# Optimization experiments

Measured on AMD Instinct MI355X. Metric: run time of the kernel, lower is better.

Reference implementation:

```python
import jax, jax.numpy as jnp
import numpy as np
from jax import lax

B = 16384  # batch; original torch module runs unbatched (1,5,27), we vectorize over B


def _conv(x, w, b, ph):
    # NCHW conv with kernel (kh,1), padding (ph,0), stride 1
    y = lax.conv_general_dilated(x, w, (1, 1), [(ph, ph), (0, 0)],
                                 dimension_numbers=('NCHW', 'OIHW', 'NCHW'))
    return y + b[None, :, None, None]


def _sl(x, w, b):
    # Semi_Linear: shared Linear applied over every (channel, height) slice ->
    # algebraically a single batched matmul on the last axis. w: (out,in)
    return jnp.einsum('bchw,ow->bcho', x, w) + b


def setup_inputs() -> dict:
    key = jax.random.key(0)
    ks = iter(jax.random.split(key, 40))
    def p(shape):
        return jax.random.normal(next(ks), shape, jnp.float32) * 0.05
    d = dict(
        x=jax.random.normal(next(ks), (B, 1, 5, 27), jnp.float32),
        w0a=p((5, 1, 3, 1)), b0a=p((5,)),
        wl0=p((18, 27)), bl0=p((18,)),
        w0b=p((25, 5, 3, 1)), b0b=p((25,)),
        w0c=p((25, 1, 1, 1)), b0c=p((25,)),
        wr0=p((18, 27)), br0=p((18,)),
        w1=p((75, 25, 2, 1)), b1=p((75,)),
        wl1=p((10, 18)), bl1=p((10,)),
        w2=p((125, 75, 2, 1)), b2=p((125,)),
        wa=p((125, 25, 3, 1)), ba=p((125,)),
        wra=p((10, 18)), bra=p((10,)),
        w0=p((300, 125, 2, 1)), b0=p((300,)),
        wl2=p((5, 10)), bl2=p((5,)),
        w0b2=p((512, 300, 2, 1)), b0b2=p((512,)),
        w0c2=p((512, 125, 3, 1)), b0c2=p((512,)),
        wr02=p((5, 10)), br02=p((5,)),
    )
    return d


def reference(x, w0a, b0a, wl0, bl0, w0b, b0b, w0c, b0c, wr0, br0,
              w1, b1, wl1, bl1, w2, b2, wa, ba, wra, bra,
              w0, b0, wl2, bl2, w0b2, b0b2, w0c2, b0c2, wr02, br02):
    # stage 0
    z = _conv(x, w0a, b0a, 1)                      # (B,5,5,27)
    z = jax.nn.relu(_sl(z, wl0, bl0))              # (B,5,5,18)
    z = _conv(z, w0b, b0b, 1)                      # (B,25,5,18)
    y = _conv(_sl(x, wr0, br0), w0c, b0c, 0)       # (B,25,5,18)
    x1 = z + y
    # stage 1
    z = _conv(x1, w1, b1, 0)                       # (B,75,4,18)
    z = jax.nn.relu(_sl(z, wl1, bl1))              # (B,75,4,10)
    z = _conv(z, w2, b2, 0)                        # (B,125,3,10)
    y = _conv(_sl(x1, wra, bra), wa, ba, 0)        # (B,125,3,10)
    x2 = z + y
    # stage 2
    z = _conv(x2, w0, b0, 0)                       # (B,300,2,10)
    z = jax.nn.relu(_sl(z, wl2, bl2))              # (B,300,2,5)
    z = _conv(z, w0b2, b0b2, 0)                    # (B,512,1,5)
    y = _conv(_sl(x2, wr02, br02), w0c2, b0c2, 0)  # (B,512,1,5)
    return z + y
```

## Files before the change

### kernel.cpp

```cpp
#include <hip/hip_runtime.h>
#include <stdint.h>


#define WB2T_OFF 0
#define WC2T_OFF 307200
#define W0T_OFF  499200
#define W1T_OFF  574200
#define WAT_OFF  577950
#define W2T_OFF  587325
#define WT_TOTAL 606075

__global__ __launch_bounds__(256)
void transpose_w(const float* __restrict__ w1, const float* __restrict__ wa,
                 const float* __restrict__ w2, const float* __restrict__ w0,
                 const float* __restrict__ wb2, const float* __restrict__ wc2,
                 float* __restrict__ ws) {
  int i = blockIdx.x * 256 + threadIdx.x;
  if (i < 3750) {
    int co = i / 50, k = i % 50;
    ws[W1T_OFF + k*75 + co] = w1[i];
  } else if (i < 13125) {
    int j = i - 3750; int co = j / 75, k = j % 75;
    ws[WAT_OFF + k*125 + co] = wa[j];
  } else if (i < 31875) {
    int j = i - 13125; int co = j / 150, k = j % 150;
    ws[W2T_OFF + k*125 + co] = w2[j];
  } else if (i < 106875) {
    int j = i - 31875; int co = j / 250, k = j % 250;
    ws[W0T_OFF + k*300 + co] = w0[j];
  } else if (i < 414075) {
    int j = i - 106875; int co = j / 600, k = j % 600;
    ws[WB2T_OFF + k*512 + co] = wb2[j];
  } else if (i < 606075) {
    int j = i - 414075; int co = j / 375, k = j % 375;
    ws[WC2T_OFF + k*512 + co] = wc2[j];
  }
}

template<int N>
__device__ __forceinline__ void ldrow(float* r, const float* p) {
  #pragma unroll
  for (int i = 0; i < N/4; ++i) {
    float4 q = reinterpret_cast<const float4*>(p)[i];
    r[4*i+0] = q.x; r[4*i+1] = q.y; r[4*i+2] = q.z; r[4*i+3] = q.w;
  }
}
template<int N>
__device__ __forceinline__ void strow(float* p, const float* r) {
  #pragma unroll
  for (int i = 0; i < N/4; ++i) {
    float4 q; q.x = r[4*i+0]; q.y = r[4*i+1]; q.z = r[4*i+2]; q.w = r[4*i+3];
    reinterpret_cast<float4*>(p)[i] = q;
  }
}

#define POOL   10112
#define X1_O   0
#define SX_O   2500
#define Z0A_O  2640
#define Z0SL_O 4500
#define T90_O  5000
#define Z1S_O  4500
#define T2_O   8100
#define X2_O   0
#define T3_O   4500
#define Z2S_O  6500

__global__ __launch_bounds__(256, 2)
void fused_net(const float* __restrict__ xg,
  const float* __restrict__ w0a_, const float* __restrict__ b0a_,
  const float* __restrict__ wl0_, const float* __restrict__ bl0_,
  const float* __restrict__ w0b_, const float* __restrict__ b0b_,
  const float* __restrict__ w0c_, const float* __restrict__ b0c_,
  const float* __restrict__ wr0_, const float* __restrict__ br0_,
  const float* __restrict__ b1_,
  const float* __restrict__ wl1_, const float* __restrict__ bl1_,
  const float* __restrict__ b2_,
  const float* __restrict__ ba_,
  const float* __restrict__ wra_, const float* __restrict__ bra_,
  const float* __restrict__ b0_,
  const float* __restrict__ wl2_, const float* __restrict__ bl2_,
  const float* __restrict__ b0b2_,
  const float* __restrict__ b0c2_,
  const float* __restrict__ wr02_,const float* __restrict__ br02_,
  const float* __restrict__ w1t, const float* __restrict__ wat,
  const float* __restrict__ w2t, const float* __restrict__ w0t,
  const float* __restrict__ wb2t, const float* __restrict__ wc2t,
  float* __restrict__ outg, int Btot)
{
  __shared__ __align__(16) float S[2*POOL];
  const int tid = threadIdx.x;
  const int b0 = blockIdx.x * 2;

  for (int i = tid; i < 270; i += 256) {
    int samp = i / 135, j = i % 135;
    int h = j / 27, w = j % 27;
    float v = 0.f;
    if (b0 + samp < Btot) v = xg[(size_t)(b0 + samp) * 135 + j];
    S[samp*POOL + SX_O + h*28 + w] = v;
  }
  __syncthreads();

  if (tid < 50) {
    int samp = tid / 25, r = tid % 25, co = r / 5, h = r % 5;
    float* P = S + samp*POOL;
    float acc[28];
    float bias = b0a_[co];
    #pragma unroll
    for (int w = 0; w < 28; ++w) acc[w] = bias;
    #pragma unroll
    for (int dh = 0; dh < 3; ++dh) {
      int hi = h + dh - 1;
      if (hi >= 0 && hi < 5) {
        float wf = w0a_[co*3 + dh];
        float row[28]; ldrow<28>(row, P + SX_O + hi*28);
        #pragma unroll
        for (int w = 0; w < 27; ++w) acc[w] += row[w] * wf;
      }
    }
    strow<28>(P + Z0A_O + (co*5 + h)*28, acc);
  }
  __syncthreads();

  if (tid < 180) {
    int samp = tid / 90, r = tid % 90;
    float* P = S + samp*POOL;
    if (r < 75) {
      int c = r / 15, q = r % 15, h = q / 3, o0 = (q % 3) * 6;
      float row[28]; ldrow<28>(row, P + Z0A_O + (c*5 + h)*28);
      float acc[6];
      #pragma unroll
      for (int k = 0; k < 6; ++k) acc[k] = bl0_[o0 + k];
      for (int w = 0; w < 27; ++w) {
        float rv = row[w];
        #pragma unroll
        for (int k = 0; k < 6; ++k) acc[k] += rv * wl0_[(o0 + k)*27 + w];
      }
      float* dst = P + Z0SL_O + (c*5 + h)*20 + o0;
      #pragma unroll
      for (int k = 0; k < 6; ++k) dst[k] = fmaxf(acc[k], 0.f);
    } else {
      int q = r - 75, h = q / 3, o0 = (q % 3) * 6;
      float row[28]; ldrow<28>(row, P + SX_O + h*28);
      float acc[6];
      #pragma unroll
      for (int k = 0; k < 6; ++k) acc[k] = br0_[o0 + k];
      for (int w = 0; w < 27; ++w) {
        float rv = row[w];
        #pragma unroll
        for (int k = 0; k < 6; ++k) acc[k] += rv * wr0_[(o0 + k)*27 + w];
      }
      float* dst = P + T90_O + h*20 + o0;
      #pragma unroll
      for (int k = 0; k < 6; ++k) dst[k] = acc[k];
    }
  }
  __syncthreads();

  if (tid < 250) {
    int samp = tid / 125, r = tid % 125, co = r / 5, h = r % 5;
    float* P = S + samp*POOL;
    float tr[20]; ldrow<20>(tr, P + T90_O + h*20);
    float wc = w0c_[co];
    float base = b0b_[co] + b0c_[co];
    float acc[20];
    #pragma unroll
    for (int o = 0; o < 18; ++o) acc[o] = base + tr[o]*wc;
    acc[18] = 0.f; acc[19] = 0.f;
    #pragma unroll
    for (int dh = 0; dh < 3; ++dh) {
      int hi = h + dh - 1;
      if (hi >= 0 && hi < 5) {
        #pragma unroll
        for (int ci = 0; ci < 5; ++ci) {
          float wgt = w0b_[(co*5 + ci)*3 + dh];
          float row[20]; ldrow<20>(row, P + Z0SL_O + (ci*5 + hi)*20);
          #pragma unroll
          for (int o = 0; o < 18; ++o) acc[o] += row[o] * wgt;
        }
      }
    }
    strow<20>(P + X1_O + (co*5 + h)*20, acc);
  }
  __syncthreads();

  for (int t = tid; t < 850; t += 256) {
    if (t < 600) {
      int samp = t / 300, r = t % 300, co = r / 4, h = r % 4;
      float* P = S + samp*POOL;
      float z1[18];
      float bias = b1_[co];
      #pragma unroll
      for (int w = 0; w < 18; ++w) z1[w] = bias;
      for (int ci = 0; ci < 25; ++ci) {
        float wx = w1t[(ci*2 + 0)*75 + co];
        float wy = w1t[(ci*2 + 1)*75 + co];
        float r0[20], r1[20];
        ldrow<20>(r0, P + X1_O + (ci*5 + h    )*20);
        ldrow<20>(r1, P + X1_O + (ci*5 + h + 1)*20);
        #pragma unroll
        for (int w = 0; w < 18; ++w) z1[w] += r0[w]*wx + r1[w]*wy;
      }
      float out[12];
      #pragma unroll
      for (int o = 0; o < 10; ++o) {
        float acc = bl1_[o];
        #pragma unroll
        for (int w = 0; w < 18; ++w) acc += z1[w] * wl1_[o*18 + w];
        out[o] = fmaxf(acc, 0.f);
      }
      out[10] = 0.f; out[11] = 0.f;
      strow<12>(P + Z1S_O + (co*4 + h)*12, out);
    } else {
      int q = t - 600;
      int samp = q / 125, r = q % 125, c = r / 5, h = r % 5;
      float* P = S + samp*POOL;
      float row[20]; ldrow<20>(row, P + X1_O + (c*5 + h)*20);
      float out[12];
      #pragma unroll
      for (int o = 0; o < 10; ++o) {
        float acc = bra_[o];
        #pragma unroll
        for (int w = 0; w < 18; ++w) acc += row[w] * wra_[o*18 + w];
        out[o] = acc;
      }
      out[10] = 0.f; out[11] = 0.f;
      strow<12>(P + T2_O + (c*5 + h)*12, out);
    }
  }
  __syncthreads();

  if (tid < 250) {
    int samp = tid / 125, co = tid % 125;
    float* P = S + samp*POOL;
    float acc[3][10];
    float bias = b2_[co] + ba_[co];
    #pragma unroll
    for (int h = 0; h < 3; ++h)
      #pragma unroll
      for (int w = 0; w < 10; ++w) acc[h][w] = bias;
    for (int ci = 0; ci < 25; ++ci) {
      float wf0 = wat[(ci*3 + 0)*125 + co];
      float wf1 = wat[(ci*3 + 1)*125 + co];
      float wf2 = wat[(ci*3 + 2)*125 + co];
      float rr[5][12];
      #pragma unroll
      for (int hh = 0; hh < 5; ++hh) ldrow<12>(rr[hh], P + T2_O + (ci*5 + hh)*12);
      #pragma unroll
      for (int h = 0; h < 3; ++h)
        #pragma unroll
        for (int w = 0; w < 10; ++w)
          acc[h][w] += rr[h][w]*wf0 + rr[h+1][w]*wf1 + rr[h+2][w]*wf2;
    }
    #pragma unroll
    for (int h = 0; h < 3; ++h) {
      float out[12];
      #pragma unroll
      for (int w = 0; w < 10; ++w) out[w] = acc[h][w];
      out[10] = 0.f; out[11] = 0.f;
      strow<12>(P + X2_O + (co*3 + h)*12, out);
    }
  }
  __syncthreads();

  if (tid < 250) {
    int samp = tid / 125, co = tid % 125;
    float* P = S + samp*POOL;
    float acc[3][12];
    #pragma unroll
    for (int h = 0; h < 3; ++h) ldrow<12>(acc[h], P + X2_O + (co*3 + h)*12);
    for (int ci = 0; ci < 75; ++ci) {
      float wx = w2t[(ci*2 + 0)*125 + co];
      float wy = w2t[(ci*2 + 1)*125 + co];
      float rr[4][12];
      #pragma unroll
      for (int hh = 0; hh < 4; ++hh) ldrow<12>(rr[hh], P + Z1S_O + (ci*4 + hh)*12);
      #pragma unroll
      for (int h = 0; h < 3; ++h)
        #pragma unroll
        for (int w = 0; w < 10; ++w)
          acc[h][w] += rr[h][w]*wx + rr[h+1][w]*wy;
    }
    #pragma unroll
    for (int h = 0; h < 3; ++h) strow<12>(P + X2_O + (co*3 + h)*12, acc[h]);
  }
  __syncthreads();

  for (int t = tid; t < 400; t += 256) {
    if (t < 150) {
      int samp = t / 75, cot = t % 75;
      int co = cot * 4;
      float* P = S + samp*POOL;
      float acc[4][2][10];
      #pragma unroll
      for (int j = 0; j < 4; ++j) {
        float bb = b0_[co + j];
        #pragma unroll
        for (int h = 0; h < 2; ++h)
          #pragma unroll
          for (int w = 0; w < 10; ++w) acc[j][h][w] = bb;
      }
      for (int ci = 0; ci < 125; ++ci) {
        float a0[12], a1[12], a2[12];
        ldrow<12>(a0, P + X2_O + (ci*3 + 0)*12);
        ldrow<12>(a1, P + X2_O + (ci*3 + 1)*12);
        ldrow<12>(a2, P + X2_O + (ci*3 + 2)*12);
        float4 wxv = *reinterpret_cast<const float4*>(w0t + (ci*2 + 0)*300 + co);
        float4 wyv = *reinterpret_cast<const float4*>(w0t + (ci*2 + 1)*300 + co);
        float wx[4] = {wxv.x, wxv.y, wxv.z, wxv.w};
        float wy[4] = {wyv.x, wyv.y, wyv.z, wyv.w};
        #pragma unroll
        for (int j = 0; j < 4; ++j)
          #pragma unroll
          for (int w = 0; w < 10; ++w) {
            acc[j][0][w] += a0[w]*wx[j] + a1[w]*wy[j];
            acc[j][1][w] += a1[w]*wx[j] + a2[w]*wy[j];
          }
      }
      #pragma unroll
      for (int j = 0; j < 4; ++j) {
        float out[12];
        #pragma unroll
        for (int h = 0; h < 2; ++h)
          #pragma unroll
          for (int o = 0; o < 5; ++o) {
            float sacc = bl2_[o];
            #pragma unroll
            for (int w = 0; w < 10; ++w) sacc += acc[j][h][w] * wl2_[o*10 + w];
            out[h*5 + o] = fmaxf(sacc, 0.f);
          }
        out[10] = 0.f; out[11] = 0.f;
        strow<12>(P + Z2S_O + (co + j)*12, out);
      }
    } else {
      int q = t - 150;
      int samp = q / 125, c = q % 125;
      float* P = S + samp*POOL;
      float rr[3][12];
      #pragma unroll
      for (int h = 0; h < 3; ++h) ldrow<12>(rr[h], P + X2_O + (c*3 + h)*12);
      float out[16];
      #pragma unroll
      for (int h = 0; h < 3; ++h)
        #pragma unroll
        for (int o = 0; o < 5; ++o) {
          float acc = br02_[o];
          #pragma unroll
          for (int w = 0; w < 10; ++w) acc += rr[h][w] * wr02_[o*10 + w];
          out[h*5 + o] = acc;
        }
      out[15] = 0.f;
      strow<16>(P + T3_O + c*16, out);
    }
  }
  __syncthreads();

  {
    int samp = tid >> 7, coq = tid & 127;
    int co = coq * 4;
    float* P = S + samp*POOL;
    float acc[4][5];
    #pragma unroll
    for (int j = 0; j < 4; ++j) {
      float bb = b0b2_[co + j] + b0c2_[co + j];
      #pragma unroll
      for (int w = 0; w < 5; ++w) acc[j][w] = bb;
    }
    for (int ci = 0; ci < 300; ++ci) {
      float a[12]; ldrow<12>(a, P + Z2S_O + ci*12);
      float4 uxv = *reinterpret_cast<const float4*>(wb2t + (ci*2 + 0)*512 + co);
      float4 uyv = *reinterpret_cast<const float4*>(wb2t + (ci*2 + 1)*512 + co);
      float ux[4] = {uxv.x, uxv.y, uxv.z, uxv.w};
      float uy[4] = {uyv.x, uyv.y, uyv.z, uyv.w};
      #pragma unroll
      for (int j = 0; j < 4; ++j)
        #pragma unroll
        for (int w = 0; w < 5; ++w)
          acc[j][w] += a[w]*ux[j] + a[5 + w]*uy[j];
    }
    for (int ci = 0; ci < 125; ++ci) {
      float t3[16]; ldrow<16>(t3, P + T3_O + ci*16);
      float4 u0v = *reinterpret_cast<const float4*>(wc2t + (ci*3 + 0)*512 + co);
      float4 u1v = *reinterpret_cast<const float4*>(wc2t + (ci*3 + 1)*512 + co);
      float4 u2v = *reinterpret_cast<const float4*>(wc2t + (ci*3 + 2)*512 + co);
      float u0[4] = {u0v.x, u0v.y, u0v.z, u0v.w};
      float u1[4] = {u1v.x, u1v.y, u1v.z, u1v.w};
      float u2[4] = {u2v.x, u2v.y, u2v.z, u2v.w};
      #pragma unroll
      for (int j = 0; j < 4; ++j)
        #pragma unroll
        for (int w = 0; w < 5; ++w)
          acc[j][w] += t3[w]*u0[j] + t3[5 + w]*u1[j] + t3[10 + w]*u2[j];
    }
    if (b0 + samp < Btot) {
      float* ob = outg + (size_t)(b0 + samp) * 2560 + co*5;
      float flat[20];
      #pragma unroll
      for (int j = 0; j < 4; ++j)
        #pragma unroll
        for (int w = 0; w < 5; ++w) flat[j*5 + w] = acc[j][w];
      strow<20>(ob, flat);
    }
  }
}

extern "C" void kernel_launch(void* const* d_in, const int* in_sizes, int n_in,
                              void* d_out, int out_size, void* d_ws, size_t ws_size,
                              hipStream_t stream) {
  (void)in_sizes; (void)n_in; (void)ws_size;
  const float* p[31];
  for (int i = 0; i < 31; ++i) p[i] = (const float*)d_in[i];
  float* ws = (float*)d_ws;

  transpose_w<<<(WT_TOTAL + 255) / 256, 256, 0, stream>>>(
      p[11] , p[17] , p[15] , p[21] ,
      p[25] , p[27] , ws);

  int Btot = out_size / 2560;
  int nb = (Btot + 1) >> 1;
  if (nb <= 0) return;
  fused_net<<<nb, 256, 0, stream>>>(
      p[0],
      p[1],  p[2],  p[3],  p[4],  p[5],  p[6],  p[7],  p[8],  p[9],  p[10],
      p[12],
      p[13], p[14],
      p[16],
      p[18],
      p[19], p[20],
      p[22],
      p[23], p[24],
      p[26],
      p[28],
      p[29], p[30],
      ws + W1T_OFF, ws + WAT_OFF, ws + W2T_OFF, ws + W0T_OFF,
      ws + WB2T_OFF, ws + WC2T_OFF,
      (float*)d_out, Btot);
}
```

Baseline: 3.461 ms.

## Reorder kernel-height convs before Semi_Linear to shrink width and fuse stages

Since a (kh,1) conv acts only on channel and height and the Semi_Linear acts only on width, the two commute. Each stage now applies the width-reducing linear first and then runs the conv on the narrower tensor. The conv bias is folded in using precomputed row sums of the linear weights. This cuts FLOPs in the stage-0/1/2 conv-then-linear chains and merges several phases, saving syncs and LDS traffic. The cost is a new shared-memory layout with aliased regions, which needs care to stay race-free.

```diff
diff --git a/kernel.cpp b/kernel.cpp
--- a/kernel.cpp
+++ b/kernel.cpp
@@ -8,12 +8,17 @@
 #define W1T_OFF  574200
 #define WAT_OFF  577950
 #define W2T_OFF  587325
-#define WT_TOTAL 606075
+#define SUM0_OFF 606075
+#define SUM1_OFF 606093
+#define SUM2_OFF 606103
+#define WT_TOTAL 606108
 
 __global__ __launch_bounds__(256)
 void transpose_w(const float* __restrict__ w1, const float* __restrict__ wa,
                  const float* __restrict__ w2, const float* __restrict__ w0,
                  const float* __restrict__ wb2, const float* __restrict__ wc2,
+                 const float* __restrict__ wl0, const float* __restrict__ wl1,
+                 const float* __restrict__ wl2,
                  float* __restrict__ ws) {
   int i = blockIdx.x * 256 + threadIdx.x;
   if (i < 3750) {
@@ -34,6 +39,18 @@
   } else if (i < 606075) {
     int j = i - 414075; int co = j / 375, k = j % 375;
     ws[WC2T_OFF + k*512 + co] = wc2[j];
+  } else if (i < 606093) {
+    int j = i - 606075; float s = 0.f;
+    for (int w = 0; w < 27; ++w) s += wl0[j*27 + w];
+    ws[SUM0_OFF + j] = s;
+  } else if (i < 606103) {
+    int j = i - 606093; float s = 0.f;
+    for (int w = 0; w < 18; ++w) s += wl1[j*18 + w];
+    ws[SUM1_OFF + j] = s;
+  } else if (i < 606108) {
+    int j = i - 606103; float s = 0.f;
+    for (int w = 0; w < 10; ++w) s += wl2[j*10 + w];
+    ws[SUM2_OFF + j] = s;
   }
 }
 
@@ -57,14 +74,16 @@
 #define POOL   10112
 #define X1_O   0
 #define SX_O   2500
-#define Z0A_O  2640
-#define Z0SL_O 4500
-#define T90_O  5000
+#define XS0_O  2640
+#define T90_O  2740
+#define Z0SL_O 2840
+#define X1S_O  2500
 #define Z1S_O  4500
 #define T2_O   8100
 #define X2_O   0
-#define T3_O   4500
-#define Z2S_O  6500
+#define T3_O   8100
+#define X2S_O  4500
+#define Z2S_O  0
 
 __global__ __launch_bounds__(256, 2)
 void fused_net(const float* __restrict__ xg,
@@ -86,6 +105,7 @@
   const float* __restrict__ w1t, const float* __restrict__ wat,
   const float* __restrict__ w2t, const float* __restrict__ w0t,
   const float* __restrict__ wb2t, const float* __restrict__ wc2t,
+  const float* __restrict__ sums,
   float* __restrict__ outg, int Btot)
 {
   __shared__ __align__(16) float S[2*POOL];
@@ -101,64 +121,55 @@
   }
   __syncthreads();
 
+  if (tid < 30) {
+    int samp = tid / 15, r = tid % 15, h = r / 3, o0 = (r % 3) * 6;
+    float* P = S + samp*POOL;
+    float row[28]; ldrow<28>(row, P + SX_O + h*28);
+    float xs[6], t9[6];
+    #pragma unroll
+    for (int k = 0; k < 6; ++k) { xs[k] = 0.f; t9[k] = br0_[o0 + k]; }
+    for (int w = 0; w < 27; ++w) {
+      float rv = row[w];
+      #pragma unroll
+      for (int k = 0; k < 6; ++k) {
+        xs[k] += rv * wl0_[(o0 + k)*27 + w];
+        t9[k] += rv * wr0_[(o0 + k)*27 + w];
+      }
+    }
+    #pragma unroll
+    for (int k = 0; k < 6; ++k) {
+      P[XS0_O + h*20 + o0 + k] = xs[k];
+      P[T90_O + h*20 + o0 + k] = t9[k];
+    }
+  }
+  __syncthreads();
+
   if (tid < 50) {
     int samp = tid / 25, r = tid % 25, co = r / 5, h = r % 5;
     float* P = S + samp*POOL;
-    float acc[28];
-    float bias = b0a_[co];
-    #pragma unroll
-    for (int w = 0; w < 28; ++w) acc[w] = bias;
+    float acc[20];
+    float bc = b0a_[co];
+    #pragma unroll
+    for (int o = 0; o < 18; ++o) acc[o] = bc * sums[o] + bl0_[o];
+    acc[18] = 0.f; acc[19] = 0.f;
     #pragma unroll
     for (int dh = 0; dh < 3; ++dh) {
       int hi = h + dh - 1;
       if (hi >= 0 && hi < 5) {
         float wf = w0a_[co*3 + dh];
-        float row[28]; ldrow<28>(row, P + SX_O + hi*28);
-        #pragma unroll
-        for (int w = 0; w < 27; ++w) acc[w] += row[w] * wf;
-      }
-    }
-    strow<28>(P + Z0A_O + (co*5 + h)*28, acc);
-  }
-  __syncthreads();
-
-  if (tid < 180) {
-    int samp = tid / 90, r = tid % 90;
-    float* P = S + samp*POOL;
-    if (r < 75) {
-      int c = r / 15, q = r % 15, h = q / 3, o0 = (q % 3) * 6;
-      float row[28]; ldrow<28>(row, P + Z0A_O + (c*5 + h)*28);
-      float acc[6];
-      #pragma unroll
-      for (int k = 0; k < 6; ++k) acc[k] = bl0_[o0 + k];
-      for (int w = 0; w < 27; ++w) {
-        float rv = row[w];
-        #pragma unroll
-        for (int k = 0; k < 6; ++k) acc[k] += rv * wl0_[(o0 + k)*27 + w];
-      }
-      float* dst = P + Z0SL_O + (c*5 + h)*20 + o0;
-      #pragma unroll
-      for (int k = 0; k < 6; ++k) dst[k] = fmaxf(acc[k], 0.f);
-    } else {
-      int q = r - 75, h = q / 3, o0 = (q % 3) * 6;
-      float row[28]; ldrow<28>(row, P + SX_O + h*28);
-      float acc[6];
-      #pragma unroll
-      for (int k = 0; k < 6; ++k) acc[k] = br0_[o0 + k];
-      for (int w = 0; w < 27; ++w) {
-        float rv = row[w];
-        #pragma unroll
-        for (int k = 0; k < 6; ++k) acc[k] += rv * wr0_[(o0 + k)*27 + w];
-      }
-      float* dst = P + T90_O + h*20 + o0;
-      #pragma unroll
-      for (int k = 0; k < 6; ++k) dst[k] = acc[k];
-    }
+        float row[20]; ldrow<20>(row, P + XS0_O + hi*20);
+        #pragma unroll
+        for (int o = 0; o < 18; ++o) acc[o] += row[o] * wf;
+      }
+    }
+    #pragma unroll
+    for (int o = 0; o < 18; ++o) acc[o] = fmaxf(acc[o], 0.f);
+    strow<20>(P + Z0SL_O + (co*5 + h)*20, acc);
   }
   __syncthreads();
 
   if (tid < 250) {
-    int samp = tid / 125, r = tid % 125, co = r / 5, h = r % 5;
+    int samp = tid / 125, r = tid % 125, h = r / 25, co = r % 25;
     float* P = S + samp*POOL;
     float tr[20]; ldrow<20>(tr, P + T90_O + h*20);
     float wc = w0c_[co];
@@ -184,48 +195,57 @@
   }
   __syncthreads();
 
-  for (int t = tid; t < 850; t += 256) {
-    if (t < 600) {
-      int samp = t / 300, r = t % 300, co = r / 4, h = r % 4;
-      float* P = S + samp*POOL;
-      float z1[18];
-      float bias = b1_[co];
-      #pragma unroll
-      for (int w = 0; w < 18; ++w) z1[w] = bias;
-      for (int ci = 0; ci < 25; ++ci) {
-        float wx = w1t[(ci*2 + 0)*75 + co];
-        float wy = w1t[(ci*2 + 1)*75 + co];
-        float r0[20], r1[20];
-        ldrow<20>(r0, P + X1_O + (ci*5 + h    )*20);
-        ldrow<20>(r1, P + X1_O + (ci*5 + h + 1)*20);
-        #pragma unroll
-        for (int w = 0; w < 18; ++w) z1[w] += r0[w]*wx + r1[w]*wy;
-      }
+  if (tid < 250) {
+    int samp = tid / 125, r = tid % 125, h = r / 25, c = r % 25;
+    float* P = S + samp*POOL;
+    float row[20]; ldrow<20>(row, P + X1_O + (c*5 + h)*20);
+    float t2[12], x1s[12];
+    #pragma unroll
+    for (int o = 0; o < 10; ++o) {
+      float a = bra_[o], s = 0.f;
+      #pragma unroll
+      for (int w = 0; w < 18; ++w) {
+        a += row[w] * wra_[o*18 + w];
+        s += row[w] * wl1_[o*18 + w];
+      }
+      t2[o] = a; x1s[o] = s;
+    }
+    t2[10] = t2[11] = 0.f; x1s[10] = x1s[11] = 0.f;
+    strow<12>(P + T2_O  + (c*5 + h)*12, t2);
+    strow<12>(P + X1S_O + (c*5 + h)*12, x1s);
+  }
+  __syncthreads();
+
+  for (int t = tid; t < 300; t += 256) {
+    int samp = t / 150, r = t % 150, co = r >> 1, h0 = (r & 1) * 2;
+    float* P = S + samp*POOL;
+    float acc[2][10];
+    float bc = b1_[co];
+    #pragma unroll
+    for (int o = 0; o < 10; ++o) {
+      float b = bc * sums[18 + o] + bl1_[o];
+      acc[0][o] = b; acc[1][o] = b;
+    }
+    for (int ci = 0; ci < 25; ++ci) {
+      float wx = w1t[(ci*2 + 0)*75 + co];
+      float wy = w1t[(ci*2 + 1)*75 + co];
+      float r0[12], r1[12], r2[12];
+      ldrow<12>(r0, P + X1S_O + (ci*5 + h0    )*12);
+      ldrow<12>(r1, P + X1S_O + (ci*5 + h0 + 1)*12);
+      ldrow<12>(r2, P + X1S_O + (ci*5 + h0 + 2)*12);
+      #pragma unroll
+      for (int o = 0; o < 10; ++o) {
+        acc[0][o] += r0[o]*wx + r1[o]*wy;
+        acc[1][o] += r1[o]*wx + r2[o]*wy;
+      }
+    }
+    #pragma unroll
+    for (int hh = 0; hh < 2; ++hh) {
       float out[12];
       #pragma unroll
-      for (int o = 0; o < 10; ++o) {
-        float acc = bl1_[o];
-        #pragma unroll
-        for (int w = 0; w < 18; ++w) acc += z1[w] * wl1_[o*18 + w];
-        out[o] = fmaxf(acc, 0.f);
-      }
+      for (int o = 0; o < 10; ++o) out[o] = fmaxf(acc[hh][o], 0.f);
       out[10] = 0.f; out[11] = 0.f;
-      strow<12>(P + Z1S_O + (co*4 + h)*12, out);
-    } else {
-      int q = t - 600;
-      int samp = q / 125, r = q % 125, c = r / 5, h = r % 5;
-      float* P = S + samp*POOL;
-      float row[20]; ldrow<20>(row, P + X1_O + (c*5 + h)*20);
-      float out[12];
-      #pragma unroll
-      for (int o = 0; o < 10; ++o) {
-        float acc = bra_[o];
-        #pragma unroll
-        for (int w = 0; w < 18; ++w) acc += row[w] * wra_[o*18 + w];
-        out[o] = acc;
-      }
-      out[10] = 0.f; out[11] = 0.f;
-      strow<12>(P + T2_O + (c*5 + h)*12, out);
+      strow<12>(P + Z1S_O + (co*4 + h0 + hh)*12, out);
     }
   }
   __syncthreads();
@@ -252,23 +272,6 @@
         for (int w = 0; w < 10; ++w)
           acc[h][w] += rr[h][w]*wf0 + rr[h+1][w]*wf1 + rr[h+2][w]*wf2;
     }
-    #pragma unroll
-    for (int h = 0; h < 3; ++h) {
-      float out[12];
-      #pragma unroll
-      for (int w = 0; w < 10; ++w) out[w] = acc[h][w];
-      out[10] = 0.f; out[11] = 0.f;
-      strow<12>(P + X2_O + (co*3 + h)*12, out);
-    }
-  }
-  __syncthreads();
-
-  if (tid < 250) {
-    int samp = tid / 125, co = tid % 125;
-    float* P = S + samp*POOL;
-    float acc[3][12];
-    #pragma unroll
-    for (int h = 0; h < 3; ++h) ldrow<12>(acc[h], P + X2_O + (co*3 + h)*12);
     for (int ci = 0; ci < 75; ++ci) {
       float wx = w2t[(ci*2 + 0)*125 + co];
       float wy = w2t[(ci*2 + 1)*125 + co];
@@ -282,75 +285,83 @@
           acc[h][w] += rr[h][w]*wx + rr[h+1][w]*wy;
     }
     #pragma unroll
-    for (int h = 0; h < 3; ++h) strow<12>(P + X2_O + (co*3 + h)*12, acc[h]);
-  }
-  __syncthreads();
-
-  for (int t = tid; t < 400; t += 256) {
-    if (t < 150) {
-      int samp = t / 75, cot = t % 75;
-      int co = cot * 4;
-      float* P = S + samp*POOL;
-      float acc[4][2][10];
-      #pragma unroll
-      for (int j = 0; j < 4; ++j) {
-        float bb = b0_[co + j];
-        #pragma unroll
-        for (int h = 0; h < 2; ++h)
-          #pragma unroll
-          for (int w = 0; w < 10; ++w) acc[j][h][w] = bb;
-      }
-      for (int ci = 0; ci < 125; ++ci) {
-        float a0[12], a1[12], a2[12];
-        ldrow<12>(a0, P + X2_O + (ci*3 + 0)*12);
-        ldrow<12>(a1, P + X2_O + (ci*3 + 1)*12);
-        ldrow<12>(a2, P + X2_O + (ci*3 + 2)*12);
-        float4 wxv = *reinterpret_cast<const float4*>(w0t + (ci*2 + 0)*300 + co);
-        float4 wyv = *reinterpret_cast<const float4*>(w0t + (ci*2 + 1)*300 + co);
-        float wx[4] = {wxv.x, wxv.y, wxv.z, wxv.w};
-        float wy[4] = {wyv.x, wyv.y, wyv.z, wyv.w};
-        #pragma unroll
-        for (int j = 0; j < 4; ++j)
-          #pragma unroll
-          for (int w = 0; w < 10; ++w) {
-            acc[j][0][w] += a0[w]*wx[j] + a1[w]*wy[j];
-            acc[j][1][w] += a1[w]*wx[j] + a2[w]*wy[j];
-          }
-      }
-      #pragma unroll
-      for (int j = 0; j < 4; ++j) {
-        float out[12];
-        #pragma unroll
-        for (int h = 0; h < 2; ++h)
-          #pragma unroll
-          for (int o = 0; o < 5; ++o) {
-            float sacc = bl2_[o];
-            #pragma unroll
-            for (int w = 0; w < 10; ++w) sacc += acc[j][h][w] * wl2_[o*10 + w];
-            out[h*5 + o] = fmaxf(sacc, 0.f);
-          }
-        out[10] = 0.f; out[11] = 0.f;
-        strow<12>(P + Z2S_O + (co + j)*12, out);
-      }
-    } else {
-      int q = t - 150;
-      int samp = q / 125, c = q % 125;
-      float* P = S + samp*POOL;
-      float rr[3][12];
-      #pragma unroll
-      for (int h = 0; h < 3; ++h) ldrow<12>(rr[h], P + X2_O + (c*3 + h)*12);
-      float out[16];
-      #pragma unroll
-      for (int h = 0; h < 3; ++h)
+    for (int h = 0; h < 3; ++h) {
+      float out[12];
+      #pragma unroll
+      for (int w = 0; w < 10; ++w) out[w] = acc[h][w];
+      out[10] = 0.f; out[11] = 0.f;
+      strow<12>(P + X2_O + (co*3 + h)*12, out);
+    }
+  }
+  __syncthreads();
+
+  if (tid < 250) {
+    int samp = tid / 125, c = tid % 125;
+    float* P = S + samp*POOL;
+    float rr[3][12];
+    #pragma unroll
+    for (int h = 0; h < 3; ++h) ldrow<12>(rr[h], P + X2_O + (c*3 + h)*12);
+    float t3[16];
+    #pragma unroll
+    for (int h = 0; h < 3; ++h) {
+      float x2s[8];
+      #pragma unroll
+      for (int o = 0; o < 5; ++o) {
+        float a = br02_[o], s = 0.f;
+        #pragma unroll
+        for (int w = 0; w < 10; ++w) {
+          a += rr[h][w] * wr02_[o*10 + w];
+          s += rr[h][w] * wl2_[o*10 + w];
+        }
+        t3[h*5 + o] = a; x2s[o] = s;
+      }
+      x2s[5] = x2s[6] = x2s[7] = 0.f;
+      strow<8>(P + X2S_O + (c*3 + h)*8, x2s);
+    }
+    t3[15] = 0.f;
+    strow<16>(P + T3_O + c*16, t3);
+  }
+  __syncthreads();
+
+  for (int t = tid; t < 300; t += 256) {
+    int samp = t / 150, q2 = t % 150, co = q2 * 2;
+    float* P = S + samp*POOL;
+    float acc[2][2][5];
+    #pragma unroll
+    for (int j = 0; j < 2; ++j) {
+      float bc = b0_[co + j];
+      #pragma unroll
+      for (int o = 0; o < 5; ++o) {
+        float b = bc * sums[28 + o] + bl2_[o];
+        acc[j][0][o] = b; acc[j][1][o] = b;
+      }
+    }
+    for (int ci = 0; ci < 125; ++ci) {
+      float2 wxv = *reinterpret_cast<const float2*>(w0t + (ci*2 + 0)*300 + co);
+      float2 wyv = *reinterpret_cast<const float2*>(w0t + (ci*2 + 1)*300 + co);
+      float a0[8], a1[8], a2[8];
+      ldrow<8>(a0, P + X2S_O + (ci*3 + 0)*8);
+      ldrow<8>(a1, P + X2S_O + (ci*3 + 1)*8);
+      ldrow<8>(a2, P + X2S_O + (ci*3 + 2)*8);
+      float wx[2] = {wxv.x, wxv.y};
+      float wy[2] = {wyv.x, wyv.y};
+      #pragma unroll
+      for (int j = 0; j < 2; ++j)
         #pragma unroll
         for (int o = 0; o < 5; ++o) {
-          float acc = br02_[o];
-          #pragma unroll
-          for (int w = 0; w < 10; ++w) acc += rr[h][w] * wr02_[o*10 + w];
-          out[h*5 + o] = acc;
+          acc[j][0][o] += a0[o]*wx[j] + a1[o]*wy[j];
+          acc[j][1][o] += a1[o]*wx[j] + a2[o]*wy[j];
         }
-      out[15] = 0.f;
-      strow<16>(P + T3_O + c*16, out);
+    }
+    #pragma unroll
+    for (int j = 0; j < 2; ++j) {
+      float out[12];
+      #pragma unroll
+      for (int h = 0; h < 2; ++h)
+        #pragma unroll
+        for (int o = 0; o < 5; ++o) out[h*5 + o] = fmaxf(acc[j][h][o], 0.f);
+      out[10] = 0.f; out[11] = 0.f;
+      strow<12>(P + Z2S_O + (co + j)*12, out);
     }
   }
   __syncthreads();
@@ -414,11 +425,12 @@
 
   transpose_w<<<(WT_TOTAL + 255) / 256, 256, 0, stream>>>(
       p[11] , p[17] , p[15] , p[21] ,
-      p[25] , p[27] , ws);
+      p[25] , p[27] ,
+      p[3] , p[13] , p[23] , ws);
 
   int Btot = out_size / 2560;
+  if (Btot <= 0) return;
   int nb = (Btot + 1) >> 1;
-  if (nb <= 0) return;
   fused_net<<<nb, 256, 0, stream>>>(
       p[0],
       p[1],  p[2],  p[3],  p[4],  p[5],  p[6],  p[7],  p[8],  p[9],  p[10],
@@ -434,5 +446,6 @@
       p[29], p[30],
       ws + W1T_OFF, ws + WAT_OFF, ws + W2T_OFF, ws + W0T_OFF,
       ws + WB2T_OFF, ws + WC2T_OFF,
+      ws + SUM0_OFF,
       (float*)d_out, Btot);
 }
```

Result: faster. 3.075 ms (-11.2%).
